# Kernel tuning notes

Hardware: AMD Instinct MI355X
Metric: run time of the kernel (lower is better)

The kernel has to match this reference:

```python
import jax, jax.numpy as jnp
import numpy as np

T, B, IN, H, L = 128, 1024, 128, 256, 2


def setup_inputs() -> dict:
    key = jax.random.key(0)
    ks = jax.random.split(key, 9)
    s_in = 1.0 / np.sqrt(IN)
    s_h = 1.0 / np.sqrt(H)
    f32 = jnp.float32
    return {
        "x": jax.random.normal(ks[0], (T, B, IN), f32),
        "initial_state": jnp.zeros((L, B, H), f32),
        "gammas": jax.random.uniform(ks[1], (L, B, H), f32),            # FiLM scale ~U[0,1)
        "betas": jax.random.uniform(ks[2], (L, B, H), f32) * 0.1,        # FiLM shift, small
        "Wx0": (jax.random.normal(ks[3], (3 * H, IN), f32) * s_in),
        "bx0": jnp.zeros((3 * H,), f32),
        "Wh0": (jax.random.normal(ks[4], (3 * H, H), f32) * s_h),
        "bh0": jnp.zeros((3 * H,), f32),
        "Wx1": (jax.random.normal(ks[5], (3 * H, H), f32) * s_h),
        "bx1": jnp.zeros((3 * H,), f32),
        "Wh1": (jax.random.normal(ks[6], (3 * H, H), f32) * s_h),
        "bh1": jnp.zeros((3 * H,), f32),
    }


def _gru_layer(x_seq, h0, gamma, beta, Wx, bx, Wh, bh):
    # Precompute the input-side gate projections for all timesteps: [T, B, 3H]
    x_gates = jnp.einsum("tbi,gi->tbg", x_seq, Wx) + bx

    def step(h, xg_t):
        h_gates = h @ Wh.T + bh                      # [B, 3H]
        x_z, x_r, x_n = jnp.split(xg_t, 3, axis=-1)
        h_z, h_r, h_n = jnp.split(h_gates, 3, axis=-1)
        z = jax.nn.sigmoid(x_z + h_z)
        r = jax.nn.sigmoid(x_r + h_r)
        n = jnp.tanh(x_n + r * h_n)
        h_t = (1.0 - z) * n + z * h
        h_t = gamma * h_t + beta                     # FiLM affine modulation
        return h_t, h_t

    h_last, outputs = jax.lax.scan(step, h0, x_gates)
    return outputs, h_last


def reference(x, initial_state, gammas, betas,
              Wx0, bx0, Wh0, bh0, Wx1, bx1, Wh1, bh1):
    out0, h0 = _gru_layer(x, initial_state[0], gammas[0], betas[0], Wx0, bx0, Wh0, bh0)
    out1, h1 = _gru_layer(out0, initial_state[1], gammas[1], betas[1], Wx1, bx1, Wh1, bh1)
    # matches torch module: (last-layer outputs [T,B,H], per-layer final states)
    return out1, jnp.stack([h0, h1], axis=0)
```

## Files before the change

kernel.cpp:

```cpp
#include <hip/hip_runtime.h>


typedef __attribute__((ext_vector_type(8))) _Float16 half8;
typedef __attribute__((ext_vector_type(4))) float   f32x4;
typedef unsigned long long u64;

#define T_  128
#define B_  1024
#define IN_ 128
#define H_  256

#define WX0_OFF 0
#define WX0_N   (48 * 4 * 512)
#define WH0_OFF (WX0_OFF + WX0_N)
#define WH0_N   (48 * 8 * 512)
#define WX1_OFF (WH0_OFF + WH0_N)
#define WX1_N   (48 * 8 * 512)
#define WH1_OFF (WX1_OFF + WX1_N)
#define WH1_N   (48 * 8 * 512)
#define WTOT    (WH1_OFF + WH1_N)

#define H0B_OFF 1376256
#define H1B_OFF (H0B_OFF + 1048576)
#define CTR_OFF (H1B_OFF + 1048576)

#define HPAR 262144

__global__ void pack_weights_k(const float* __restrict__ Wx0, const float* __restrict__ Wh0,
                               const float* __restrict__ Wx1, const float* __restrict__ Wh1,
                               _Float16* __restrict__ wp)
{
    int p = blockIdx.x * blockDim.x + threadIdx.x;
    if (p >= WTOT) return;
    const float* src; int q, nk, K;
    if (p < WX1_OFF) {
        if (p < WH0_OFF) { src = Wx0; q = p - WX0_OFF; nk = 4; K = 128; }
        else             { src = Wh0; q = p - WH0_OFF; nk = 8; K = 256; }
    } else {
        if (p < WH1_OFF) { src = Wx1; q = p - WX1_OFF; nk = 8; K = 256; }
        else             { src = Wh1; q = p - WH1_OFF; nk = 8; K = 256; }
    }
    int chunk = q >> 9;
    int e     = q & 511;
    int nt = chunk / nk, kt = chunk - nt * nk;
    int lane = e >> 3, j = e & 7;
    int n = nt * 16 + (lane & 15);
    int k = kt * 32 + ((lane >> 4) << 3) + j;
    wp[p] = (_Float16)src[n * K + k];
}

__device__ __forceinline__ float sigmoid_(float v) { return 1.f / (1.f + __expf(-v)); }
__device__ __forceinline__ float tanh_(float v) {
    float e = __expf(2.f * v);
    return 1.f - 2.f / (e + 1.f);
}

__device__ __forceinline__ half8 cvt_h8f(f32x4 a, f32x4 b) {
    half8 r;
    r[0] = (_Float16)a[0]; r[1] = (_Float16)a[1]; r[2] = (_Float16)a[2]; r[3] = (_Float16)a[3];
    r[4] = (_Float16)b[0]; r[5] = (_Float16)b[1]; r[6] = (_Float16)b[2]; r[7] = (_Float16)b[3];
    return r;
}

__device__ __forceinline__ u64 cvt_h4(f32x4 a) {
    union { _Float16 h[4]; u64 q; } u;
    u.h[0] = (_Float16)a[0]; u.h[1] = (_Float16)a[1];
    u.h[2] = (_Float16)a[2]; u.h[3] = (_Float16)a[3];
    return u.q;
}

__device__ __forceinline__ void h8_store_xchg(_Float16* p, half8 v) {
    union { half8 h; u64 q[2]; } u; u.h = v;
    u64* q = (u64*)p;
    u64 o0 = __hip_atomic_exchange(q,     u.q[0], __ATOMIC_RELAXED, __HIP_MEMORY_SCOPE_AGENT);
    u64 o1 = __hip_atomic_exchange(q + 1, u.q[1], __ATOMIC_RELAXED, __HIP_MEMORY_SCOPE_AGENT);
    asm volatile("" :: "v"(o0), "v"(o1));
}
__device__ __forceinline__ void h4_store_xchg(_Float16* p, u64 v) {
    u64 o = __hip_atomic_exchange((u64*)p, v, __ATOMIC_RELAXED, __HIP_MEMORY_SCOPE_AGENT);
    asm volatile("" :: "v"(o));
}

#define MFMA(a, b, c) __builtin_amdgcn_mfma_f32_16x16x32_f16((a), (b), (c), 0, 0, 0)


__device__ __forceinline__ void bg_barrier(int* c, int target) {
    __syncthreads();
    if (threadIdx.x == 0) {
        __hip_atomic_fetch_add(c, 1, __ATOMIC_RELAXED, __HIP_MEMORY_SCOPE_AGENT);
        while (__hip_atomic_load(c, __ATOMIC_RELAXED, __HIP_MEMORY_SCOPE_AGENT) < target)
            __builtin_amdgcn_s_sleep(1);
        (void)__hip_atomic_load(c, __ATOMIC_ACQUIRE, __HIP_MEMORY_SCOPE_AGENT);
    }
    __syncthreads();
}

__launch_bounds__(256, 1)
__global__ void film_gru_k(const float* __restrict__ x,
                           const float* __restrict__ h_init,
                           const float* __restrict__ gammas,
                           const float* __restrict__ betas,
                           const float* __restrict__ bx0, const float* __restrict__ bh0,
                           const float* __restrict__ bx1, const float* __restrict__ bh1,
                           const _Float16* __restrict__ wp,
                           _Float16* __restrict__ h0b,
                           _Float16* __restrict__ h1b,
                           int* __restrict__ ctr,
                           float* __restrict__ out)
{
    __shared__ __align__(16) _Float16 wlds[84 * 512];
    __shared__ __align__(16) float bounce[4][16 * 24];

    const int tid  = threadIdx.x;
    const int w    = tid >> 6;
    const int lane = tid & 63;
    const int l15  = lane & 15;
    const int lq   = lane >> 4;
    const int bg   = blockIdx.x & 15;
    const int cg   = blockIdx.x >> 4;
    const int b0   = bg * 64;
    const int rowbase = b0 + w * 16;
    const int col  = cg * 16 + l15;

    int* bctr = ctr + bg * 32;

    for (int i = tid; i < 84 * 64; i += 256) {
        int c = i >> 6, e = i & 63;
        size_t src;
        if (c < 12)      { int g = c >> 2;   int kt = c & 3;  src = WX0_OFF + (size_t)(((g*16 + cg)*4) + kt) * 512; }
        else if (c < 36) { int q = c - 12;   int g = q >> 3;  int kt = q & 7; src = WH0_OFF + (size_t)(((g*16 + cg)*8) + kt) * 512; }
        else if (c < 60) { int q = c - 36;   int g = q >> 3;  int kt = q & 7; src = WX1_OFF + (size_t)(((g*16 + cg)*8) + kt) * 512; }
        else             { int q = c - 60;   int g = q >> 3;  int kt = q & 7; src = WH1_OFF + (size_t)(((g*16 + cg)*8) + kt) * 512; }
        *(half8*)&wlds[(size_t)c * 512 + (size_t)e * 8] = *(const half8*)(wp + src + (size_t)e * 8);
    }

    float bz0 = bx0[col] + bh0[col];
    float br0 = bx0[256 + col] + bh0[256 + col];
    float bxn0 = bx0[512 + col], bhn0 = bh0[512 + col];
    float bz1 = bx1[col] + bh1[col];
    float br1 = bx1[256 + col] + bh1[256 + col];
    float bxn1 = bx1[512 + col], bhn1 = bh1[512 + col];

    float g0v[4], be0v[4], g1v[4], be1v[4], hr0[4], hr1[4];
    #pragma unroll
    for (int g = 0; g < 4; g++) {
        size_t row = rowbase + lq * 4 + g;
        size_t gi = row * H_ + col;
        g0v[g] = gammas[gi];              be0v[g] = betas[gi];
        g1v[g] = gammas[(size_t)B_ * H_ + gi]; be1v[g] = betas[(size_t)B_ * H_ + gi];
        hr0[g] = h_init[gi];
        hr1[g] = h_init[(size_t)B_ * H_ + gi];
    }

    const int mykt   = cg >> 1;
    const int lhalf  = (cg & 1) * 32;
    const size_t mychunk = ((size_t)(bg * 4 + w) * 8 + mykt) * 512;
    if (lane < 32) {
        int row = lane & 15, ch = lane >> 4;
        const float* s0 = h_init + (size_t)(rowbase + row) * H_ + cg * 16 + ch * 8;
        half8 v0 = cvt_h8f(*(const f32x4*)s0, *(const f32x4*)(s0 + 4));
        const float* s1 = s0 + (size_t)B_ * H_;
        half8 v1 = cvt_h8f(*(const f32x4*)s1, *(const f32x4*)(s1 + 4));
        size_t d = mychunk + (size_t)(lhalf + lane) * 8;
        h8_store_xchg(&h0b[d], v0);
        h8_store_xchg(&h1b[d], v1);
        h8_store_xchg(&h1b[HPAR + d], v1);
    }

    int epoch = 0;
    bg_barrier(bctr, 16 * (++epoch));

    const f32x4 zero4 = {0.f, 0.f, 0.f, 0.f};
    const size_t hchunkbase = (size_t)(bg * 4 + w) * 8 * 512;

    const int st_row  = (lane >> 1) & 15;
    const int st_coff = ((lane >> 5) << 3) + ((lane & 1) << 2);
    const size_t st_elem = mychunk + (size_t)lhalf * 8 + (size_t)lane * 4;

    f32x4 xr[8];
    {
        const float* xb = x + (size_t)(rowbase + l15) * IN_ + lq * 8;
        #pragma unroll
        for (int kt = 0; kt < 4; kt++) {
            xr[2*kt]   = *(const f32x4*)(xb + kt * 32);
            xr[2*kt+1] = *(const f32x4*)(xb + kt * 32 + 4);
        }
    }

    for (int k = 0; k <= T_; k++) {
        const int rp = k & 1, wpar = rp ^ 1;

        const _Float16* o0r = h0b + (size_t)rp * HPAR + hchunkbase + (size_t)lane * 8;
        const _Float16* h1r = h1b + (size_t)rp * HPAR + hchunkbase + (size_t)lane * 8;
        half8 a0c[8], a1[8];
        #pragma unroll
        for (int kt = 0; kt < 8; kt++) a0c[kt] = *(const half8*)(o0r + (size_t)kt * 512);
        #pragma unroll
        for (int kt = 0; kt < 8; kt++) a1[kt] = *(const half8*)(h1r + (size_t)kt * 512);

        if (k < T_) {
            f32x4 az = zero4, ar = zero4, axn = zero4, ahn = zero4;
            #pragma unroll
            for (int kt = 0; kt < 4; kt++) {
                half8 a = cvt_h8f(xr[2*kt], xr[2*kt+1]);
                az  = MFMA(a, *(const half8*)&wlds[(0*4 + kt) * 512 + lane * 8], az);
                ar  = MFMA(a, *(const half8*)&wlds[(1*4 + kt) * 512 + lane * 8], ar);
                axn = MFMA(a, *(const half8*)&wlds[(2*4 + kt) * 512 + lane * 8], axn);
            }
            #pragma unroll
            for (int kt = 0; kt < 8; kt++) {
                az  = MFMA(a0c[kt], *(const half8*)&wlds[(12 + 0*8 + kt) * 512 + lane * 8], az);
                ar  = MFMA(a0c[kt], *(const half8*)&wlds[(12 + 1*8 + kt) * 512 + lane * 8], ar);
                ahn = MFMA(a0c[kt], *(const half8*)&wlds[(12 + 2*8 + kt) * 512 + lane * 8], ahn);
            }

            {
                int tn = (k + 1 < T_) ? k + 1 : k;
                const float* xb = x + (size_t)tn * B_ * IN_ + (size_t)(rowbase + l15) * IN_ + lq * 8;
                #pragma unroll
                for (int kt = 0; kt < 4; kt++) {
                    xr[2*kt]   = *(const f32x4*)(xb + kt * 32);
                    xr[2*kt+1] = *(const f32x4*)(xb + kt * 32 + 4);
                }
            }

            #pragma unroll
            for (int g = 0; g < 4; g++) {
                float z = sigmoid_(az[g] + bz0);
                float r = sigmoid_(ar[g] + br0);
                float n = tanh_(axn[g] + bxn0 + r * (ahn[g] + bhn0));
                float h = (1.f - z) * n + z * hr0[g];
                h = g0v[g] * h + be0v[g];
                hr0[g] = h;
                bounce[w][(lq * 4 + g) * 24 + l15] = h;
            }
            {
                f32x4 v = *(const f32x4*)&bounce[w][st_row * 24 + st_coff];
                h4_store_xchg(&h0b[(size_t)wpar * HPAR + st_elem], cvt_h4(v));
            }
        }

        if (k >= 1) {
            f32x4 az = zero4, ar = zero4, axn = zero4, ahn = zero4;
            #pragma unroll
            for (int kt = 0; kt < 8; kt++) {
                az  = MFMA(a0c[kt], *(const half8*)&wlds[(36 + 0*8 + kt) * 512 + lane * 8], az);
                ar  = MFMA(a0c[kt], *(const half8*)&wlds[(36 + 1*8 + kt) * 512 + lane * 8], ar);
                axn = MFMA(a0c[kt], *(const half8*)&wlds[(36 + 2*8 + kt) * 512 + lane * 8], axn);
            }
            #pragma unroll
            for (int kt = 0; kt < 8; kt++) {
                az  = MFMA(a1[kt], *(const half8*)&wlds[(60 + 0*8 + kt) * 512 + lane * 8], az);
                ar  = MFMA(a1[kt], *(const half8*)&wlds[(60 + 1*8 + kt) * 512 + lane * 8], ar);
                ahn = MFMA(a1[kt], *(const half8*)&wlds[(60 + 2*8 + kt) * 512 + lane * 8], ahn);
            }

            #pragma unroll
            for (int g = 0; g < 4; g++) {
                float z = sigmoid_(az[g] + bz1);
                float r = sigmoid_(ar[g] + br1);
                float n = tanh_(axn[g] + bxn1 + r * (ahn[g] + bhn1));
                float h = (1.f - z) * n + z * hr1[g];
                h = g1v[g] * h + be1v[g];
                hr1[g] = h;
                bounce[w][(lq * 4 + g) * 24 + l15] = h;
            }
            {
                int row = lane >> 2, coff = (lane & 3) * 4;
                f32x4 v = *(const f32x4*)&bounce[w][row * 24 + coff];
                *(f32x4*)&out[(size_t)(k-1) * B_ * H_ + (size_t)(rowbase + row) * H_ + cg * 16 + coff] = v;
            }
            {
                f32x4 v = *(const f32x4*)&bounce[w][st_row * 24 + st_coff];
                h4_store_xchg(&h1b[(size_t)wpar * HPAR + st_elem], cvt_h4(v));
            }
        }

        if (k < T_) bg_barrier(bctr, 16 * (++epoch));
    }

    size_t base = (size_t)T_ * B_ * H_;
    #pragma unroll
    for (int g = 0; g < 4; g++) {
        size_t row = rowbase + lq * 4 + g;
        out[base + row * H_ + col] = hr0[g];
        out[base + (size_t)B_ * H_ + row * H_ + col] = hr1[g];
    }
}

extern "C" void kernel_launch(void* const* d_in, const int* in_sizes, int n_in,
                              void* d_out, int out_size, void* d_ws, size_t ws_size,
                              hipStream_t stream)
{
    const float* x    = (const float*)d_in[0];
    const float* hini = (const float*)d_in[1];
    const float* gam  = (const float*)d_in[2];
    const float* bet  = (const float*)d_in[3];
    const float* Wx0  = (const float*)d_in[4];
    const float* bx0  = (const float*)d_in[5];
    const float* Wh0  = (const float*)d_in[6];
    const float* bh0  = (const float*)d_in[7];
    const float* Wx1  = (const float*)d_in[8];
    const float* bx1  = (const float*)d_in[9];
    const float* Wh1  = (const float*)d_in[10];
    const float* bh1  = (const float*)d_in[11];

    _Float16* wp  = (_Float16*)d_ws;
    _Float16* h0b = (_Float16*)((char*)d_ws + H0B_OFF);
    _Float16* h1b = (_Float16*)((char*)d_ws + H1B_OFF);
    int*      ctr = (int*)((char*)d_ws + CTR_OFF);
    float*    outp = (float*)d_out;

    hipMemsetAsync(ctr, 0, 16 * 32 * sizeof(int), stream);
    pack_weights_k<<<WTOT / 256, 256, 0, stream>>>(Wx0, Wh0, Wx1, Wh1, wp);

    void* args[] = { (void*)&x, (void*)&hini, (void*)&gam, (void*)&bet,
                     (void*)&bx0, (void*)&bh0, (void*)&bx1, (void*)&bh1,
                     (void*)&wp, (void*)&h0b, (void*)&h1b, (void*)&ctr, (void*)&outp };
    hipLaunchCooperativeKernel((void*)film_gru_k, dim3(256), dim3(256),
                               args, 0, stream);
}
```

Measured before the change: 984.7 us.

## Split layer-0 and layer-1 work into separate wave roles with per-wave barrier

```diff
diff --git a/kernel.cpp b/kernel.cpp
--- a/kernel.cpp
+++ b/kernel.cpp
@@ -95,7 +95,19 @@
     __syncthreads();
 }
 
-__launch_bounds__(256, 1)
+__device__ __forceinline__ void wave_arrive_wait(int* c, int* wcnt, int t8last, int t16) {
+    asm volatile("s_waitcnt vmcnt(0)" ::: "memory");
+    if ((threadIdx.x & 63) == 0) {
+        int old = __hip_atomic_fetch_add(wcnt, 1, __ATOMIC_RELAXED, __HIP_MEMORY_SCOPE_WORKGROUP);
+        if (old == t8last)
+            __hip_atomic_fetch_add(c, 1, __ATOMIC_RELAXED, __HIP_MEMORY_SCOPE_AGENT);
+        while (__hip_atomic_load(c, __ATOMIC_RELAXED, __HIP_MEMORY_SCOPE_AGENT) < t16)
+            __builtin_amdgcn_s_sleep(1);
+    }
+    (void)__hip_atomic_load(c, __ATOMIC_ACQUIRE, __HIP_MEMORY_SCOPE_AGENT);
+}
+
+__launch_bounds__(512, 1)
 __global__ void film_gru_k(const float* __restrict__ x,
                            const float* __restrict__ h_init,
                            const float* __restrict__ gammas,
@@ -109,22 +121,26 @@
                            float* __restrict__ out)
 {
     __shared__ __align__(16) _Float16 wlds[84 * 512];
-    __shared__ __align__(16) float bounce[4][16 * 24];
+    __shared__ __align__(16) float bounce[8][16 * 24];
+    __shared__ int warr;
 
     const int tid  = threadIdx.x;
     const int w    = tid >> 6;
+    const int wr   = w & 3;
+    const int role = w >> 2;
     const int lane = tid & 63;
     const int l15  = lane & 15;
     const int lq   = lane >> 4;
     const int bg   = blockIdx.x & 15;
     const int cg   = blockIdx.x >> 4;
     const int b0   = bg * 64;
-    const int rowbase = b0 + w * 16;
+    const int rowbase = b0 + wr * 16;
     const int col  = cg * 16 + l15;
 
     int* bctr = ctr + bg * 32;
-
-    for (int i = tid; i < 84 * 64; i += 256) {
+    if (tid == 0) warr = 0;
+
+    for (int i = tid; i < 84 * 64; i += 512) {
         int c = i >> 6, e = i & 63;
         size_t src;
         if (c < 12)      { int g = c >> 2;   int kt = c & 3;  src = WX0_OFF + (size_t)(((g*16 + cg)*4) + kt) * 512; }
@@ -134,51 +150,48 @@
         *(half8*)&wlds[(size_t)c * 512 + (size_t)e * 8] = *(const half8*)(wp + src + (size_t)e * 8);
     }
 
-    float bz0 = bx0[col] + bh0[col];
-    float br0 = bx0[256 + col] + bh0[256 + col];
-    float bxn0 = bx0[512 + col], bhn0 = bh0[512 + col];
-    float bz1 = bx1[col] + bh1[col];
-    float br1 = bx1[256 + col] + bh1[256 + col];
-    float bxn1 = bx1[512 + col], bhn1 = bh1[512 + col];
-
-    float g0v[4], be0v[4], g1v[4], be1v[4], hr0[4], hr1[4];
+    const float* bxP = role ? bx1 : bx0;
+    const float* bhP = role ? bh1 : bh0;
+    const size_t roff = (size_t)role * B_ * H_;
+    float bz  = bxP[col] + bhP[col];
+    float br  = bxP[256 + col] + bhP[256 + col];
+    float bxn = bxP[512 + col], bhn = bhP[512 + col];
+
+    float gv[4], bev[4], hr[4];
     #pragma unroll
     for (int g = 0; g < 4; g++) {
         size_t row = rowbase + lq * 4 + g;
-        size_t gi = row * H_ + col;
-        g0v[g] = gammas[gi];              be0v[g] = betas[gi];
-        g1v[g] = gammas[(size_t)B_ * H_ + gi]; be1v[g] = betas[(size_t)B_ * H_ + gi];
-        hr0[g] = h_init[gi];
-        hr1[g] = h_init[(size_t)B_ * H_ + gi];
+        size_t gi = roff + row * H_ + col;
+        gv[g] = gammas[gi]; bev[g] = betas[gi]; hr[g] = h_init[gi];
     }
 
     const int mykt   = cg >> 1;
     const int lhalf  = (cg & 1) * 32;
-    const size_t mychunk = ((size_t)(bg * 4 + w) * 8 + mykt) * 512;
+    const size_t mychunk = ((size_t)(bg * 4 + wr) * 8 + mykt) * 512;
     if (lane < 32) {
-        int row = lane & 15, ch = lane >> 4;
-        const float* s0 = h_init + (size_t)(rowbase + row) * H_ + cg * 16 + ch * 8;
-        half8 v0 = cvt_h8f(*(const f32x4*)s0, *(const f32x4*)(s0 + 4));
-        const float* s1 = s0 + (size_t)B_ * H_;
-        half8 v1 = cvt_h8f(*(const f32x4*)s1, *(const f32x4*)(s1 + 4));
+        int prow = lane & 15, pch = lane >> 4;
+        const float* s = h_init + roff + (size_t)(rowbase + prow) * H_ + cg * 16 + pch * 8;
+        half8 v = cvt_h8f(*(const f32x4*)s, *(const f32x4*)(s + 4));
         size_t d = mychunk + (size_t)(lhalf + lane) * 8;
-        h8_store_xchg(&h0b[d], v0);
-        h8_store_xchg(&h1b[d], v1);
-        h8_store_xchg(&h1b[HPAR + d], v1);
-    }
-
-    int epoch = 0;
-    bg_barrier(bctr, 16 * (++epoch));
+        if (role == 0) {
+            h8_store_xchg(&h0b[d], v);
+        } else {
+            h8_store_xchg(&h1b[d], v);
+            h8_store_xchg(&h1b[HPAR + d], v);
+        }
+    }
+
+    bg_barrier(bctr, 16);
 
     const f32x4 zero4 = {0.f, 0.f, 0.f, 0.f};
-    const size_t hchunkbase = (size_t)(bg * 4 + w) * 8 * 512;
+    const size_t hchunkbase = (size_t)(bg * 4 + wr) * 8 * 512;
 
     const int st_row  = (lane >> 1) & 15;
     const int st_coff = ((lane >> 5) << 3) + ((lane & 1) << 2);
     const size_t st_elem = mychunk + (size_t)lhalf * 8 + (size_t)lane * 4;
 
     f32x4 xr[8];
-    {
+    if (role == 0) {
         const float* xb = x + (size_t)(rowbase + l15) * IN_ + lq * 8;
         #pragma unroll
         for (int kt = 0; kt < 4; kt++) {
@@ -190,101 +203,110 @@
     for (int k = 0; k <= T_; k++) {
         const int rp = k & 1, wpar = rp ^ 1;
 
-        const _Float16* o0r = h0b + (size_t)rp * HPAR + hchunkbase + (size_t)lane * 8;
-        const _Float16* h1r = h1b + (size_t)rp * HPAR + hchunkbase + (size_t)lane * 8;
-        half8 a0c[8], a1[8];
-        #pragma unroll
-        for (int kt = 0; kt < 8; kt++) a0c[kt] = *(const half8*)(o0r + (size_t)kt * 512);
-        #pragma unroll
-        for (int kt = 0; kt < 8; kt++) a1[kt] = *(const half8*)(h1r + (size_t)kt * 512);
-
-        if (k < T_) {
-            f32x4 az = zero4, ar = zero4, axn = zero4, ahn = zero4;
-            #pragma unroll
-            for (int kt = 0; kt < 4; kt++) {
-                half8 a = cvt_h8f(xr[2*kt], xr[2*kt+1]);
-                az  = MFMA(a, *(const half8*)&wlds[(0*4 + kt) * 512 + lane * 8], az);
-                ar  = MFMA(a, *(const half8*)&wlds[(1*4 + kt) * 512 + lane * 8], ar);
-                axn = MFMA(a, *(const half8*)&wlds[(2*4 + kt) * 512 + lane * 8], axn);
+        if (role == 0) {
+            if (k < T_) {
+                const _Float16* o0r = h0b + (size_t)rp * HPAR + hchunkbase + (size_t)lane * 8;
+                half8 a0c[8];
+                #pragma unroll
+                for (int kt = 0; kt < 8; kt++) a0c[kt] = *(const half8*)(o0r + (size_t)kt * 512);
+
+                f32x4 az = zero4, ar = zero4, axn = zero4, ahn = zero4;
+                #pragma unroll
+                for (int kt = 0; kt < 4; kt++) {
+                    half8 a = cvt_h8f(xr[2*kt], xr[2*kt+1]);
+                    az  = MFMA(a, *(const half8*)&wlds[(0*4 + kt) * 512 + lane * 8], az);
+                    ar  = MFMA(a, *(const half8*)&wlds[(1*4 + kt) * 512 + lane * 8], ar);
+                    axn = MFMA(a, *(const half8*)&wlds[(2*4 + kt) * 512 + lane * 8], axn);
+                }
+                #pragma unroll
+                for (int kt = 0; kt < 8; kt++) {
+                    az  = MFMA(a0c[kt], *(const half8*)&wlds[(12 + 0*8 + kt) * 512 + lane * 8], az);
+                    ar  = MFMA(a0c[kt], *(const half8*)&wlds[(12 + 1*8 + kt) * 512 + lane * 8], ar);
+                    ahn = MFMA(a0c[kt], *(const half8*)&wlds[(12 + 2*8 + kt) * 512 + lane * 8], ahn);
+                }
+
+                {
+                    int tn = (k + 1 < T_) ? k + 1 : k;
+                    const float* xb = x + (size_t)tn * B_ * IN_ + (size_t)(rowbase + l15) * IN_ + lq * 8;
+                    #pragma unroll
+                    for (int kt = 0; kt < 4; kt++) {
+                        xr[2*kt]   = *(const f32x4*)(xb + kt * 32);
+                        xr[2*kt+1] = *(const f32x4*)(xb + kt * 32 + 4);
+                    }
+                }
+
+                #pragma unroll
+                for (int g = 0; g < 4; g++) {
+                    float z = sigmoid_(az[g] + bz);
+                    float r = sigmoid_(ar[g] + br);
+                    float n = tanh_(axn[g] + bxn + r * (ahn[g] + bhn));
+                    float h = (1.f - z) * n + z * hr[g];
+                    h = gv[g] * h + bev[g];
+                    hr[g] = h;
+                    bounce[w][(lq * 4 + g) * 24 + l15] = h;
+                }
+                {
+                    f32x4 v = *(const f32x4*)&bounce[w][st_row * 24 + st_coff];
+                    h4_store_xchg(&h0b[(size_t)wpar * HPAR + st_elem], cvt_h4(v));
+                }
             }
-            #pragma unroll
-            for (int kt = 0; kt < 8; kt++) {
-                az  = MFMA(a0c[kt], *(const half8*)&wlds[(12 + 0*8 + kt) * 512 + lane * 8], az);
-                ar  = MFMA(a0c[kt], *(const half8*)&wlds[(12 + 1*8 + kt) * 512 + lane * 8], ar);
-                ahn = MFMA(a0c[kt], *(const half8*)&wlds[(12 + 2*8 + kt) * 512 + lane * 8], ahn);
-            }
-
-            {
-                int tn = (k + 1 < T_) ? k + 1 : k;
-                const float* xb = x + (size_t)tn * B_ * IN_ + (size_t)(rowbase + l15) * IN_ + lq * 8;
-                #pragma unroll
-                for (int kt = 0; kt < 4; kt++) {
-                    xr[2*kt]   = *(const f32x4*)(xb + kt * 32);
-                    xr[2*kt+1] = *(const f32x4*)(xb + kt * 32 + 4);
-                }
-            }
-
-            #pragma unroll
-            for (int g = 0; g < 4; g++) {
-                float z = sigmoid_(az[g] + bz0);
-                float r = sigmoid_(ar[g] + br0);
-                float n = tanh_(axn[g] + bxn0 + r * (ahn[g] + bhn0));
-                float h = (1.f - z) * n + z * hr0[g];
-                h = g0v[g] * h + be0v[g];
-                hr0[g] = h;
-                bounce[w][(lq * 4 + g) * 24 + l15] = h;
-            }
-            {
-                f32x4 v = *(const f32x4*)&bounce[w][st_row * 24 + st_coff];
-                h4_store_xchg(&h0b[(size_t)wpar * HPAR + st_elem], cvt_h4(v));
+        } else {
+            if (k >= 1) {
+                const _Float16* o0r = h0b + (size_t)rp * HPAR + hchunkbase + (size_t)lane * 8;
+                const _Float16* h1r = h1b + (size_t)rp * HPAR + hchunkbase + (size_t)lane * 8;
+                half8 a0c[8], a1[8];
+                #pragma unroll
+                for (int kt = 0; kt < 8; kt++) a0c[kt] = *(const half8*)(o0r + (size_t)kt * 512);
+                #pragma unroll
+                for (int kt = 0; kt < 8; kt++) a1[kt] = *(const half8*)(h1r + (size_t)kt * 512);
+
+                f32x4 az = zero4, ar = zero4, axn = zero4, ahn = zero4;
+                #pragma unroll
+                for (int kt = 0; kt < 8; kt++) {
+                    az  = MFMA(a0c[kt], *(const half8*)&wlds[(36 + 0*8 + kt) * 512 + lane * 8], az);
+                    ar  = MFMA(a0c[kt], *(const half8*)&wlds[(36 + 1*8 + kt) * 512 + lane * 8], ar);
+                    axn = MFMA(a0c[kt], *(const half8*)&wlds[(36 + 2*8 + kt) * 512 + lane * 8], axn);
+                }
+                #pragma unroll
+                for (int kt = 0; kt < 8; kt++) {
+                    az  = MFMA(a1[kt], *(const half8*)&wlds[(60 + 0*8 + kt) * 512 + lane * 8], az);
+                    ar  = MFMA(a1[kt], *(const half8*)&wlds[(60 + 1*8 + kt) * 512 + lane * 8], ar);
+                    ahn = MFMA(a1[kt], *(const half8*)&wlds[(60 + 2*8 + kt) * 512 + lane * 8], ahn);
+                }
+
+                #pragma unroll
+                for (int g = 0; g < 4; g++) {
+                    float z = sigmoid_(az[g] + bz);
+                    float r = sigmoid_(ar[g] + br);
+                    float n = tanh_(axn[g] + bxn + r * (ahn[g] + bhn));
+                    float h = (1.f - z) * n + z * hr[g];
+                    h = gv[g] * h + bev[g];
+                    hr[g] = h;
+                    bounce[w][(lq * 4 + g) * 24 + l15] = h;
+                }
+                {
+                    int prow = lane >> 2, pcoff = (lane & 3) * 4;
+                    f32x4 v = *(const f32x4*)&bounce[w][prow * 24 + pcoff];
+                    *(f32x4*)&out[(size_t)(k-1) * B_ * H_ + (size_t)(rowbase + prow) * H_ + cg * 16 + pcoff] = v;
+                }
+                {
+                    f32x4 v = *(const f32x4*)&bounce[w][st_row * 24 + st_coff];
+                    h4_store_xchg(&h1b[(size_t)wpar * HPAR + st_elem], cvt_h4(v));
+                }
             }
         }
 
-        if (k >= 1) {
-            f32x4 az = zero4, ar = zero4, axn = zero4, ahn = zero4;
-            #pragma unroll
-            for (int kt = 0; kt < 8; kt++) {
-                az  = MFMA(a0c[kt], *(const half8*)&wlds[(36 + 0*8 + kt) * 512 + lane * 8], az);
-                ar  = MFMA(a0c[kt], *(const half8*)&wlds[(36 + 1*8 + kt) * 512 + lane * 8], ar);
-                axn = MFMA(a0c[kt], *(const half8*)&wlds[(36 + 2*8 + kt) * 512 + lane * 8], axn);
-            }
-            #pragma unroll
-            for (int kt = 0; kt < 8; kt++) {
-                az  = MFMA(a1[kt], *(const half8*)&wlds[(60 + 0*8 + kt) * 512 + lane * 8], az);
-                ar  = MFMA(a1[kt], *(const half8*)&wlds[(60 + 1*8 + kt) * 512 + lane * 8], ar);
-                ahn = MFMA(a1[kt], *(const half8*)&wlds[(60 + 2*8 + kt) * 512 + lane * 8], ahn);
-            }
-
-            #pragma unroll
-            for (int g = 0; g < 4; g++) {
-                float z = sigmoid_(az[g] + bz1);
-                float r = sigmoid_(ar[g] + br1);
-                float n = tanh_(axn[g] + bxn1 + r * (ahn[g] + bhn1));
-                float h = (1.f - z) * n + z * hr1[g];
-                h = g1v[g] * h + be1v[g];
-                hr1[g] = h;
-                bounce[w][(lq * 4 + g) * 24 + l15] = h;
-            }
-            {
-                int row = lane >> 2, coff = (lane & 3) * 4;
-                f32x4 v = *(const f32x4*)&bounce[w][row * 24 + coff];
-                *(f32x4*)&out[(size_t)(k-1) * B_ * H_ + (size_t)(rowbase + row) * H_ + cg * 16 + coff] = v;
-            }
-            {
-                f32x4 v = *(const f32x4*)&bounce[w][st_row * 24 + st_coff];
-                h4_store_xchg(&h1b[(size_t)wpar * HPAR + st_elem], cvt_h4(v));
-            }
+        if (k < T_) {
+            int n = k + 1;
+            wave_arrive_wait(bctr, &warr, 8 * n - 1, 16 * (n + 1));
         }
-
-        if (k < T_) bg_barrier(bctr, 16 * (++epoch));
-    }
-
-    size_t base = (size_t)T_ * B_ * H_;
+    }
+
+    size_t base = (size_t)T_ * B_ * H_ + roff;
     #pragma unroll
     for (int g = 0; g < 4; g++) {
         size_t row = rowbase + lq * 4 + g;
-        out[base + row * H_ + col] = hr0[g];
-        out[base + (size_t)B_ * H_ + row * H_ + col] = hr1[g];
+        out[base + row * H_ + col] = hr[g];
     }
 }
 
@@ -317,6 +339,6 @@
     void* args[] = { (void*)&x, (void*)&hini, (void*)&gam, (void*)&bet,
                      (void*)&bx0, (void*)&bh0, (void*)&bx1, (void*)&bh1,
                      (void*)&wp, (void*)&h0b, (void*)&h1b, (void*)&ctr, (void*)&outp };
-    hipLaunchCooperativeKernel((void*)film_gru_k, dim3(256), dim3(256),
+    hipLaunchCooperativeKernel((void*)film_gru_k, dim3(256), dim3(512),
                                args, 0, stream);
 }
```

Result: slower. 2.640 ms (+168.1%).

## Split per-step group barrier into separate layer-0 and layer-1 arrive/wait counters

Applied to the files above, without the earlier changes.

```diff
diff --git a/kernel.cpp b/kernel.cpp
--- a/kernel.cpp
+++ b/kernel.cpp
@@ -84,15 +84,25 @@
 #define MFMA(a, b, c) __builtin_amdgcn_mfma_f32_16x16x32_f16((a), (b), (c), 0, 0, 0)
 
 
-__device__ __forceinline__ void bg_barrier(int* c, int target) {
-    __syncthreads();
+__device__ __forceinline__ void wait_acquire(int* c, int target) {
     if (threadIdx.x == 0) {
-        __hip_atomic_fetch_add(c, 1, __ATOMIC_RELAXED, __HIP_MEMORY_SCOPE_AGENT);
         while (__hip_atomic_load(c, __ATOMIC_RELAXED, __HIP_MEMORY_SCOPE_AGENT) < target)
             __builtin_amdgcn_s_sleep(1);
         (void)__hip_atomic_load(c, __ATOMIC_ACQUIRE, __HIP_MEMORY_SCOPE_AGENT);
     }
     __syncthreads();
+}
+__device__ __forceinline__ void wait_relaxed(int* c, int target) {
+    if (threadIdx.x == 0) {
+        while (__hip_atomic_load(c, __ATOMIC_RELAXED, __HIP_MEMORY_SCOPE_AGENT) < target)
+            __builtin_amdgcn_s_sleep(1);
+    }
+    __syncthreads();
+}
+__device__ __forceinline__ void arrive(int* c) {
+    __syncthreads();
+    if (threadIdx.x == 0)
+        __hip_atomic_fetch_add(c, 1, __ATOMIC_RELAXED, __HIP_MEMORY_SCOPE_AGENT);
 }
 
 __launch_bounds__(256, 1)
@@ -123,6 +133,9 @@
     const int col  = cg * 16 + l15;
 
     int* bctr = ctr + bg * 32;
+    int* c0   = bctr;
+    int* c1   = bctr + 1;
+    int* c2   = bctr + 16;
 
     for (int i = tid; i < 84 * 64; i += 256) {
         int c = i >> 6, e = i & 63;
@@ -156,8 +169,8 @@
     const int lhalf  = (cg & 1) * 32;
     const size_t mychunk = ((size_t)(bg * 4 + w) * 8 + mykt) * 512;
     if (lane < 32) {
-        int row = lane & 15, ch = lane >> 4;
-        const float* s0 = h_init + (size_t)(rowbase + row) * H_ + cg * 16 + ch * 8;
+        int prow = lane & 15, pch = lane >> 4;
+        const float* s0 = h_init + (size_t)(rowbase + prow) * H_ + cg * 16 + pch * 8;
         half8 v0 = cvt_h8f(*(const f32x4*)s0, *(const f32x4*)(s0 + 4));
         const float* s1 = s0 + (size_t)B_ * H_;
         half8 v1 = cvt_h8f(*(const f32x4*)s1, *(const f32x4*)(s1 + 4));
@@ -167,8 +180,8 @@
         h8_store_xchg(&h1b[HPAR + d], v1);
     }
 
-    int epoch = 0;
-    bg_barrier(bctr, 16 * (++epoch));
+    arrive(c0);
+    wait_acquire(c0, 16);
 
     const f32x4 zero4 = {0.f, 0.f, 0.f, 0.f};
     const size_t hchunkbase = (size_t)(bg * 4 + w) * 8 * 512;
@@ -189,16 +202,14 @@
 
     for (int k = 0; k <= T_; k++) {
         const int rp = k & 1, wpar = rp ^ 1;
-
-        const _Float16* o0r = h0b + (size_t)rp * HPAR + hchunkbase + (size_t)lane * 8;
-        const _Float16* h1r = h1b + (size_t)rp * HPAR + hchunkbase + (size_t)lane * 8;
-        half8 a0c[8], a1[8];
-        #pragma unroll
-        for (int kt = 0; kt < 8; kt++) a0c[kt] = *(const half8*)(o0r + (size_t)kt * 512);
-        #pragma unroll
-        for (int kt = 0; kt < 8; kt++) a1[kt] = *(const half8*)(h1r + (size_t)kt * 512);
+        half8 a0c[8];
 
         if (k < T_) {
+            if (k > 0) wait_acquire(c1, 16 * k);
+            const _Float16* o0r = h0b + (size_t)rp * HPAR + hchunkbase + (size_t)lane * 8;
+            #pragma unroll
+            for (int kt = 0; kt < 8; kt++) a0c[kt] = *(const half8*)(o0r + (size_t)kt * 512);
+
             f32x4 az = zero4, ar = zero4, axn = zero4, ahn = zero4;
             #pragma unroll
             for (int kt = 0; kt < 4; kt++) {
@@ -238,9 +249,22 @@
                 f32x4 v = *(const f32x4*)&bounce[w][st_row * 24 + st_coff];
                 h4_store_xchg(&h0b[(size_t)wpar * HPAR + st_elem], cvt_h4(v));
             }
+            arrive(c1);
         }
 
         if (k >= 1) {
+            if (k > 1) wait_relaxed(c2, 16 * (k - 1));
+            if (k == T_) {
+                wait_acquire(c1, 16 * T_);
+                const _Float16* o0r = h0b + (size_t)rp * HPAR + hchunkbase + (size_t)lane * 8;
+                #pragma unroll
+                for (int kt = 0; kt < 8; kt++) a0c[kt] = *(const half8*)(o0r + (size_t)kt * 512);
+            }
+            const _Float16* h1r = h1b + (size_t)rp * HPAR + hchunkbase + (size_t)lane * 8;
+            half8 a1[8];
+            #pragma unroll
+            for (int kt = 0; kt < 8; kt++) a1[kt] = *(const half8*)(h1r + (size_t)kt * 512);
+
             f32x4 az = zero4, ar = zero4, axn = zero4, ahn = zero4;
             #pragma unroll
             for (int kt = 0; kt < 8; kt++) {
@@ -266,17 +290,16 @@
                 bounce[w][(lq * 4 + g) * 24 + l15] = h;
             }
             {
-                int row = lane >> 2, coff = (lane & 3) * 4;
-                f32x4 v = *(const f32x4*)&bounce[w][row * 24 + coff];
-                *(f32x4*)&out[(size_t)(k-1) * B_ * H_ + (size_t)(rowbase + row) * H_ + cg * 16 + coff] = v;
+                int prow = lane >> 2, pcoff = (lane & 3) * 4;
+                f32x4 v = *(const f32x4*)&bounce[w][prow * 24 + pcoff];
+                *(f32x4*)&out[(size_t)(k-1) * B_ * H_ + (size_t)(rowbase + prow) * H_ + cg * 16 + pcoff] = v;
             }
             {
                 f32x4 v = *(const f32x4*)&bounce[w][st_row * 24 + st_coff];
                 h4_store_xchg(&h1b[(size_t)wpar * HPAR + st_elem], cvt_h4(v));
             }
+            arrive(c2);
         }
-
-        if (k < T_) bg_barrier(bctr, 16 * (++epoch));
     }
 
     size_t base = (size_t)T_ * B_ * H_;
```

New measurement: 1.238 ms. 25.7% more time.
